# Optimization experiments

Measured on AMD Instinct MI355X. Metric: run time of the kernel, lower is better.

## Reference

```python
import jax, jax.numpy as jnp
import numpy as np

BATCH = 4096
INPUT_SIZE = 512
MAX_TERMS = 8
NUM_HEADS = 4
KERNEL_SIZE = 8  # must equal MAX_TERMS for the original module's math to be consistent
LN_EPS = 1e-5


def setup_inputs() -> dict:
    key = jax.random.key(0)
    k = jax.random.split(key, 6)
    x = jax.random.normal(k[0], (BATCH, INPUT_SIZE), dtype=jnp.float32)
    scale_param = jnp.ones((INPUT_SIZE,), dtype=jnp.float32)
    # ParameterList of num_heads tensors -> stacked along leading head dim
    poly_weights = jax.random.normal(k[1], (NUM_HEADS, INPUT_SIZE, MAX_TERMS), dtype=jnp.float32)
    kernels = jax.random.normal(k[2], (NUM_HEADS, INPUT_SIZE, MAX_TERMS, KERNEL_SIZE), dtype=jnp.float32)
    ln_gamma = jnp.ones((INPUT_SIZE * MAX_TERMS * NUM_HEADS,), dtype=jnp.float32)
    ln_beta = jnp.zeros((INPUT_SIZE * MAX_TERMS * NUM_HEADS,), dtype=jnp.float32)
    return {"x": x, "scale_param": scale_param, "poly_weights": poly_weights,
            "kernels": kernels, "ln_gamma": ln_gamma, "ln_beta": ln_beta}


def reference(x, scale_param, poly_weights, kernels, ln_gamma, ln_beta):
    b = x.shape[0]
    m = kernels.shape[2]  # max_terms
    xs = x * scale_param  # [b, i]
    # Chebyshev recurrence T_0..T_{m-1}; small fixed-length Python loop
    Ts = [jnp.ones_like(xs), xs]
    for _ in range(2, m):
        Ts.append(2.0 * xs * Ts[-1] - Ts[-2])
    x_cheb = jnp.stack(Ts, axis=-1)  # [b, i, m]
    # per-feature batched matmul over all heads at once: [b,h,i,k]
    x_head = jnp.einsum('bim,himk->bhik', x_cheb, kernels)
    # poly_weights broadcast (valid since k == m)
    x_head = x_head * poly_weights[None]  # [b,h,i,k]
    x_head = jax.nn.silu(x_head)
    # torch concatenates per-head flats along dim 1 -> (h, i, k) ordering
    flat = x_head.reshape(b, -1)  # [b, h*i*k]
    # LayerNorm (biased variance, eps=1e-5) over full feature dim
    mean = jnp.mean(flat, axis=-1, keepdims=True)
    var = jnp.mean(jnp.square(flat - mean), axis=-1, keepdims=True)
    out = (flat - mean) * jax.lax.rsqrt(var + LN_EPS) * ln_gamma + ln_beta
    return out
```

## Files before the change

### kernel.cpp

```cpp
#include <hip/hip_runtime.h>

#define BATCH 4096
#define ISZ   512
#define MT    8
#define NH    4
#define KS    8
#define NFEAT (NH * ISZ * KS)
#define LN_EPS 1e-5f

typedef float vfloat4 __attribute__((ext_vector_type(4)));

__global__ void prep_w2(const float* __restrict__ kern, const float* __restrict__ poly,
                        float* __restrict__ W2) {
    int dst = blockIdx.x * 256 + threadIdx.x;
    int l = dst & 3;
    int t = (dst >> 2) & 511;
    int q = (dst >> 11) & 7;
    int j = dst >> 14;
    int c = q >> 1;
    int m = (q & 1) * 4 + l;
    int f = j * 2048 + t * 4 + c;
    W2[dst] = kern[(f >> 3) * 64 + m * 8 + (f & 7)] * poly[f];
}

__device__ __forceinline__ float dot8(float4 w0, float4 w1, float4 a0, float4 a1) {
    return w0.x*a0.x + w0.y*a0.y + w0.z*a0.z + w0.w*a0.w
         + w1.x*a1.x + w1.y*a1.y + w1.z*a1.z + w1.w*a1.w;
}

__device__ __forceinline__ float fast_silu(float d) {
    return d * __builtin_amdgcn_rcpf(1.f + __expf(-d));
}

__device__ __forceinline__ void cheb_basis(float xs, float4& a0, float4& a1) {
    float t2x = xs + xs;
    a0.x = 1.f;
    a0.y = xs;
    a0.z = t2x * a0.y - a0.x;
    a0.w = t2x * a0.z - a0.y;
    a1.x = t2x * a0.w - a0.z;
    a1.y = t2x * a1.x - a0.w;
    a1.z = t2x * a1.y - a1.x;
    a1.w = t2x * a1.z - a1.y;
}

template <bool USE_W2>
__global__ __launch_bounds__(512)
void cheb_main(const float* __restrict__ x, const float* __restrict__ scale,
               const float4* __restrict__ W2v, const float* __restrict__ kern,
               const float* __restrict__ poly,
               const float* __restrict__ gamma, const float* __restrict__ beta,
               float* __restrict__ out) {
    __shared__ float xs[2][ISZ];
    __shared__ float red[8][4];

    const int t  = threadIdx.x;
    const int r0 = blockIdx.x * 2;

    for (int idx = t; idx < 2 * ISZ; idx += 512) {
        int r = idx >> 9, i = idx & 511;
        xs[r][i] = x[(r0 + r) * ISZ + i] * scale[i];
    }
    __syncthreads();

    float sum0 = 0.f, sq0 = 0.f, sum1 = 0.f, sq1 = 0.f;
    #pragma unroll
    for (int j = 0; j < 8; ++j) {
        const int i = (j * 256 + (t >> 1)) & 511;
        float4 wa[8];
        if (USE_W2) {
            #pragma unroll
            for (int q = 0; q < 8; ++q) wa[q] = W2v[(j * 8 + q) * 512 + t];
        } else {
            #pragma unroll
            for (int c = 0; c < 4; ++c) {
                const int f = j * 2048 + t * 4 + c;
                const float p = poly[f];
                const int base = (f >> 3) * 64 + (f & 7);
                wa[2*c]   = make_float4(kern[base]*p,    kern[base+8]*p,
                                        kern[base+16]*p, kern[base+24]*p);
                wa[2*c+1] = make_float4(kern[base+32]*p, kern[base+40]*p,
                                        kern[base+48]*p, kern[base+56]*p);
            }
        }
        float xa = xs[0][i], xb = xs[1][i];
        float4 a0, a1, b0, b1;
        cheb_basis(xa, a0, a1);
        cheb_basis(xb, b0, b1);
        #pragma unroll
        for (int c = 0; c < 4; ++c) {
            float s0 = fast_silu(dot8(wa[2*c], wa[2*c+1], a0, a1));
            float s1 = fast_silu(dot8(wa[2*c], wa[2*c+1], b0, b1));
            sum0 += s0; sq0 += s0 * s0;
            sum1 += s1; sq1 += s1 * s1;
        }
    }

    #pragma unroll
    for (int off = 32; off > 0; off >>= 1) {
        sum0 += __shfl_xor(sum0, off, 64);
        sq0  += __shfl_xor(sq0,  off, 64);
        sum1 += __shfl_xor(sum1, off, 64);
        sq1  += __shfl_xor(sq1,  off, 64);
    }
    const int wave = t >> 6;
    if ((t & 63) == 0) {
        red[wave][0] = sum0; red[wave][1] = sq0;
        red[wave][2] = sum1; red[wave][3] = sq1;
    }
    __syncthreads();

    float ts0 = 0.f, tq0 = 0.f, ts1 = 0.f, tq1 = 0.f;
    #pragma unroll
    for (int wv = 0; wv < 8; ++wv) {
        ts0 += red[wv][0]; tq0 += red[wv][1];
        ts1 += red[wv][2]; tq1 += red[wv][3];
    }
    const float invN = 1.f / (float)NFEAT;
    const float mean0 = ts0 * invN, mean1 = ts1 * invN;
    const float rs0 = rsqrtf(fmaxf(tq0 * invN - mean0 * mean0, 0.f) + LN_EPS);
    const float rs1 = rsqrtf(fmaxf(tq1 * invN - mean1 * mean1, 0.f) + LN_EPS);

    float* o0 = out + (size_t)r0 * NFEAT;
    float* o1 = o0 + NFEAT;
    #pragma unroll
    for (int j = 0; j < 8; ++j) {
        const int i  = (j * 256 + (t >> 1)) & 511;
        const int f0 = j * 2048 + t * 4;
        float4 wa[8];
        if (USE_W2) {
            #pragma unroll
            for (int q = 0; q < 8; ++q) wa[q] = W2v[(j * 8 + q) * 512 + t];
        } else {
            #pragma unroll
            for (int c = 0; c < 4; ++c) {
                const int f = f0 + c;
                const float p = poly[f];
                const int base = (f >> 3) * 64 + (f & 7);
                wa[2*c]   = make_float4(kern[base]*p,    kern[base+8]*p,
                                        kern[base+16]*p, kern[base+24]*p);
                wa[2*c+1] = make_float4(kern[base+32]*p, kern[base+40]*p,
                                        kern[base+48]*p, kern[base+56]*p);
            }
        }
        float xa = xs[0][i], xb = xs[1][i];
        float4 a0, a1, b0, b1;
        cheb_basis(xa, a0, a1);
        cheb_basis(xb, b0, b1);
        float4 g  = *(const float4*)(gamma + f0);
        float4 bb = *(const float4*)(beta  + f0);
        vfloat4 r0v, r1v;
        {
            float s;
            s = fast_silu(dot8(wa[0], wa[1], a0, a1));
            r0v.x = (s - mean0) * rs0 * g.x + bb.x;
            s = fast_silu(dot8(wa[2], wa[3], a0, a1));
            r0v.y = (s - mean0) * rs0 * g.y + bb.y;
            s = fast_silu(dot8(wa[4], wa[5], a0, a1));
            r0v.z = (s - mean0) * rs0 * g.z + bb.z;
            s = fast_silu(dot8(wa[6], wa[7], a0, a1));
            r0v.w = (s - mean0) * rs0 * g.w + bb.w;

            s = fast_silu(dot8(wa[0], wa[1], b0, b1));
            r1v.x = (s - mean1) * rs1 * g.x + bb.x;
            s = fast_silu(dot8(wa[2], wa[3], b0, b1));
            r1v.y = (s - mean1) * rs1 * g.y + bb.y;
            s = fast_silu(dot8(wa[4], wa[5], b0, b1));
            r1v.z = (s - mean1) * rs1 * g.z + bb.z;
            s = fast_silu(dot8(wa[6], wa[7], b0, b1));
            r1v.w = (s - mean1) * rs1 * g.w + bb.w;
        }
        __builtin_nontemporal_store(r0v, (vfloat4*)(o0 + f0));
        __builtin_nontemporal_store(r1v, (vfloat4*)(o1 + f0));
    }
}

extern "C" void kernel_launch(void* const* d_in, const int* in_sizes, int n_in,
                              void* d_out, int out_size, void* d_ws, size_t ws_size,
                              hipStream_t stream) {
    const float* x     = (const float*)d_in[0];
    const float* scale = (const float*)d_in[1];
    const float* poly  = (const float*)d_in[2];
    const float* kern  = (const float*)d_in[3];
    const float* gamma = (const float*)d_in[4];
    const float* beta  = (const float*)d_in[5];
    float* out = (float*)d_out;

    const size_t W2_BYTES = (size_t)NFEAT * 8 * sizeof(float);
    if (ws_size >= W2_BYTES) {
        float* W2 = (float*)d_ws;
        prep_w2<<<(NFEAT * 8) / 256, 256, 0, stream>>>(kern, poly, W2);
        cheb_main<true><<<BATCH / 2, 512, 0, stream>>>(x, scale, (const float4*)W2,
                                                       kern, poly, gamma, beta, out);
    } else {
        cheb_main<false><<<BATCH / 2, 512, 0, stream>>>(x, scale, nullptr,
                                                        kern, poly, gamma, beta, out);
    }
}
```

Before: 356.5 us.

## Convert Chebyshev weights to monomial form, use Horner, process four rows per block

```diff
diff --git a/kernel.cpp b/kernel.cpp
--- a/kernel.cpp
+++ b/kernel.cpp
@@ -7,66 +7,81 @@
 #define KS    8
 #define NFEAT (NH * ISZ * KS)
 #define LN_EPS 1e-5f
+#define ROWS  4
 
 typedef float vfloat4 __attribute__((ext_vector_type(4)));
 
+__device__ __forceinline__ void cheb2mono(const float w[8], float4& m0, float4& m1) {
+    m0.x = w[0] - w[2] + w[4] - w[6];
+    m0.y = w[1] - 3.f*w[3] + 5.f*w[5] - 7.f*w[7];
+    m0.z = 2.f*w[2] - 8.f*w[4] + 18.f*w[6];
+    m0.w = 4.f*w[3] - 20.f*w[5] + 56.f*w[7];
+    m1.x = 8.f*w[4] - 48.f*w[6];
+    m1.y = 16.f*w[5] - 112.f*w[7];
+    m1.z = 32.f*w[6];
+    m1.w = 64.f*w[7];
+}
+
 __global__ void prep_w2(const float* __restrict__ kern, const float* __restrict__ poly,
-                        float* __restrict__ W2) {
-    int dst = blockIdx.x * 256 + threadIdx.x;
-    int l = dst & 3;
-    int t = (dst >> 2) & 511;
-    int q = (dst >> 11) & 7;
-    int j = dst >> 14;
-    int c = q >> 1;
-    int m = (q & 1) * 4 + l;
-    int f = j * 2048 + t * 4 + c;
-    W2[dst] = kern[(f >> 3) * 64 + m * 8 + (f & 7)] * poly[f];
-}
-
-__device__ __forceinline__ float dot8(float4 w0, float4 w1, float4 a0, float4 a1) {
-    return w0.x*a0.x + w0.y*a0.y + w0.z*a0.z + w0.w*a0.w
-         + w1.x*a1.x + w1.y*a1.y + w1.z*a1.z + w1.w*a1.w;
+                        float4* __restrict__ W2) {
+    const int f = blockIdx.x * 256 + threadIdx.x;
+    const int j = f >> 11;
+    const int t = (f >> 2) & 511;
+    const int c = f & 3;
+    const int base = (f >> 3) * 64 + (f & 7);
+    const float p = poly[f];
+    float w[8];
+    #pragma unroll
+    for (int m = 0; m < 8; ++m) w[m] = kern[base + m * 8] * p;
+    float4 m0, m1;
+    cheb2mono(w, m0, m1);
+    W2[(j * 8 + 2 * c    ) * 512 + t] = m0;
+    W2[(j * 8 + 2 * c + 1) * 512 + t] = m1;
 }
 
 __device__ __forceinline__ float fast_silu(float d) {
     return d * __builtin_amdgcn_rcpf(1.f + __expf(-d));
 }
 
-__device__ __forceinline__ void cheb_basis(float xs, float4& a0, float4& a1) {
-    float t2x = xs + xs;
-    a0.x = 1.f;
-    a0.y = xs;
-    a0.z = t2x * a0.y - a0.x;
-    a0.w = t2x * a0.z - a0.y;
-    a1.x = t2x * a0.w - a0.z;
-    a1.y = t2x * a1.x - a0.w;
-    a1.z = t2x * a1.y - a1.x;
-    a1.w = t2x * a1.z - a1.y;
+__device__ __forceinline__ float horner8(float4 w0, float4 w1, float x) {
+    float s = w1.w;
+    s = fmaf(s, x, w1.z);
+    s = fmaf(s, x, w1.y);
+    s = fmaf(s, x, w1.x);
+    s = fmaf(s, x, w0.w);
+    s = fmaf(s, x, w0.z);
+    s = fmaf(s, x, w0.y);
+    s = fmaf(s, x, w0.x);
+    return s;
 }
 
 template <bool USE_W2>
-__global__ __launch_bounds__(512)
+__global__ __launch_bounds__(512, 4)
 void cheb_main(const float* __restrict__ x, const float* __restrict__ scale,
                const float4* __restrict__ W2v, const float* __restrict__ kern,
                const float* __restrict__ poly,
                const float* __restrict__ gamma, const float* __restrict__ beta,
                float* __restrict__ out) {
-    __shared__ float xs[2][ISZ];
-    __shared__ float red[8][4];
+    __shared__ float xs[ROWS][ISZ];
+    __shared__ float red[8][2 * ROWS];
 
     const int t  = threadIdx.x;
-    const int r0 = blockIdx.x * 2;
-
-    for (int idx = t; idx < 2 * ISZ; idx += 512) {
-        int r = idx >> 9, i = idx & 511;
+    const int r0 = blockIdx.x * ROWS;
+
+    #pragma unroll
+    for (int idx = t; idx < ROWS * ISZ; idx += 512) {
+        const int r = idx >> 9, i = idx & 511;
         xs[r][i] = x[(r0 + r) * ISZ + i] * scale[i];
     }
     __syncthreads();
 
-    float sum0 = 0.f, sq0 = 0.f, sum1 = 0.f, sq1 = 0.f;
+    float sum[ROWS], sq[ROWS];
+    #pragma unroll
+    for (int r = 0; r < ROWS; ++r) { sum[r] = 0.f; sq[r] = 0.f; }
+
     #pragma unroll
     for (int j = 0; j < 8; ++j) {
-        const int i = (j * 256 + (t >> 1)) & 511;
+        const int i = ((j & 1) << 8) + (t >> 1);
         float4 wa[8];
         if (USE_W2) {
             #pragma unroll
@@ -75,57 +90,63 @@
             #pragma unroll
             for (int c = 0; c < 4; ++c) {
                 const int f = j * 2048 + t * 4 + c;
+                const int base = (f >> 3) * 64 + (f & 7);
                 const float p = poly[f];
-                const int base = (f >> 3) * 64 + (f & 7);
-                wa[2*c]   = make_float4(kern[base]*p,    kern[base+8]*p,
-                                        kern[base+16]*p, kern[base+24]*p);
-                wa[2*c+1] = make_float4(kern[base+32]*p, kern[base+40]*p,
-                                        kern[base+48]*p, kern[base+56]*p);
-            }
-        }
-        float xa = xs[0][i], xb = xs[1][i];
-        float4 a0, a1, b0, b1;
-        cheb_basis(xa, a0, a1);
-        cheb_basis(xb, b0, b1);
+                float w[8];
+                #pragma unroll
+                for (int m = 0; m < 8; ++m) w[m] = kern[base + m * 8] * p;
+                cheb2mono(w, wa[2 * c], wa[2 * c + 1]);
+            }
+        }
+        float xv[ROWS];
+        #pragma unroll
+        for (int r = 0; r < ROWS; ++r) xv[r] = xs[r][i];
         #pragma unroll
         for (int c = 0; c < 4; ++c) {
-            float s0 = fast_silu(dot8(wa[2*c], wa[2*c+1], a0, a1));
-            float s1 = fast_silu(dot8(wa[2*c], wa[2*c+1], b0, b1));
-            sum0 += s0; sq0 += s0 * s0;
-            sum1 += s1; sq1 += s1 * s1;
+            #pragma unroll
+            for (int r = 0; r < ROWS; ++r) {
+                const float s = fast_silu(horner8(wa[2 * c], wa[2 * c + 1], xv[r]));
+                sum[r] += s;
+                sq[r]   = fmaf(s, s, sq[r]);
+            }
         }
     }
 
     #pragma unroll
     for (int off = 32; off > 0; off >>= 1) {
-        sum0 += __shfl_xor(sum0, off, 64);
-        sq0  += __shfl_xor(sq0,  off, 64);
-        sum1 += __shfl_xor(sum1, off, 64);
-        sq1  += __shfl_xor(sq1,  off, 64);
+        #pragma unroll
+        for (int r = 0; r < ROWS; ++r) {
+            sum[r] += __shfl_xor(sum[r], off, 64);
+            sq[r]  += __shfl_xor(sq[r],  off, 64);
+        }
     }
     const int wave = t >> 6;
     if ((t & 63) == 0) {
-        red[wave][0] = sum0; red[wave][1] = sq0;
-        red[wave][2] = sum1; red[wave][3] = sq1;
+        #pragma unroll
+        for (int r = 0; r < ROWS; ++r) {
+            red[wave][r]        = sum[r];
+            red[wave][ROWS + r] = sq[r];
+        }
     }
     __syncthreads();
 
-    float ts0 = 0.f, tq0 = 0.f, ts1 = 0.f, tq1 = 0.f;
-    #pragma unroll
-    for (int wv = 0; wv < 8; ++wv) {
-        ts0 += red[wv][0]; tq0 += red[wv][1];
-        ts1 += red[wv][2]; tq1 += red[wv][3];
-    }
-    const float invN = 1.f / (float)NFEAT;
-    const float mean0 = ts0 * invN, mean1 = ts1 * invN;
-    const float rs0 = rsqrtf(fmaxf(tq0 * invN - mean0 * mean0, 0.f) + LN_EPS);
-    const float rs1 = rsqrtf(fmaxf(tq1 * invN - mean1 * mean1, 0.f) + LN_EPS);
-
-    float* o0 = out + (size_t)r0 * NFEAT;
-    float* o1 = o0 + NFEAT;
+    float rs[ROWS], nm[ROWS];
+    {
+        const float invN = 1.f / (float)NFEAT;
+        #pragma unroll
+        for (int r = 0; r < ROWS; ++r) {
+            float ts = 0.f, tq = 0.f;
+            #pragma unroll
+            for (int wv = 0; wv < 8; ++wv) { ts += red[wv][r]; tq += red[wv][ROWS + r]; }
+            const float mean = ts * invN;
+            rs[r] = rsqrtf(fmaxf(tq * invN - mean * mean, 0.f) + LN_EPS);
+            nm[r] = -mean * rs[r];
+        }
+    }
+
     #pragma unroll
     for (int j = 0; j < 8; ++j) {
-        const int i  = (j * 256 + (t >> 1)) & 511;
+        const int i  = ((j & 1) << 8) + (t >> 1);
         const int f0 = j * 2048 + t * 4;
         float4 wa[8];
         if (USE_W2) {
@@ -135,43 +156,34 @@
             #pragma unroll
             for (int c = 0; c < 4; ++c) {
                 const int f = f0 + c;
+                const int base = (f >> 3) * 64 + (f & 7);
                 const float p = poly[f];
-                const int base = (f >> 3) * 64 + (f & 7);
-                wa[2*c]   = make_float4(kern[base]*p,    kern[base+8]*p,
-                                        kern[base+16]*p, kern[base+24]*p);
-                wa[2*c+1] = make_float4(kern[base+32]*p, kern[base+40]*p,
-                                        kern[base+48]*p, kern[base+56]*p);
-            }
-        }
-        float xa = xs[0][i], xb = xs[1][i];
-        float4 a0, a1, b0, b1;
-        cheb_basis(xa, a0, a1);
-        cheb_basis(xb, b0, b1);
-        float4 g  = *(const float4*)(gamma + f0);
-        float4 bb = *(const float4*)(beta  + f0);
-        vfloat4 r0v, r1v;
-        {
-            float s;
-            s = fast_silu(dot8(wa[0], wa[1], a0, a1));
-            r0v.x = (s - mean0) * rs0 * g.x + bb.x;
-            s = fast_silu(dot8(wa[2], wa[3], a0, a1));
-            r0v.y = (s - mean0) * rs0 * g.y + bb.y;
-            s = fast_silu(dot8(wa[4], wa[5], a0, a1));
-            r0v.z = (s - mean0) * rs0 * g.z + bb.z;
-            s = fast_silu(dot8(wa[6], wa[7], a0, a1));
-            r0v.w = (s - mean0) * rs0 * g.w + bb.w;
-
-            s = fast_silu(dot8(wa[0], wa[1], b0, b1));
-            r1v.x = (s - mean1) * rs1 * g.x + bb.x;
-            s = fast_silu(dot8(wa[2], wa[3], b0, b1));
-            r1v.y = (s - mean1) * rs1 * g.y + bb.y;
-            s = fast_silu(dot8(wa[4], wa[5], b0, b1));
-            r1v.z = (s - mean1) * rs1 * g.z + bb.z;
-            s = fast_silu(dot8(wa[6], wa[7], b0, b1));
-            r1v.w = (s - mean1) * rs1 * g.w + bb.w;
-        }
-        __builtin_nontemporal_store(r0v, (vfloat4*)(o0 + f0));
-        __builtin_nontemporal_store(r1v, (vfloat4*)(o1 + f0));
+                float w[8];
+                #pragma unroll
+                for (int m = 0; m < 8; ++m) w[m] = kern[base + m * 8] * p;
+                cheb2mono(w, wa[2 * c], wa[2 * c + 1]);
+            }
+        }
+        float xv[ROWS];
+        #pragma unroll
+        for (int r = 0; r < ROWS; ++r) xv[r] = xs[r][i];
+        const float4 g  = *(const float4*)(gamma + f0);
+        const float4 bb = *(const float4*)(beta  + f0);
+        vfloat4 rv[ROWS];
+        #pragma unroll
+        for (int c = 0; c < 4; ++c) {
+            const float gc = (c == 0) ? g.x  : (c == 1) ? g.y  : (c == 2) ? g.z  : g.w;
+            const float bc = (c == 0) ? bb.x : (c == 1) ? bb.y : (c == 2) ? bb.z : bb.w;
+            #pragma unroll
+            for (int r = 0; r < ROWS; ++r) {
+                const float s = fast_silu(horner8(wa[2 * c], wa[2 * c + 1], xv[r]));
+                rv[r][c] = fmaf(fmaf(s, rs[r], nm[r]), gc, bc);
+            }
+        }
+        #pragma unroll
+        for (int r = 0; r < ROWS; ++r)
+            __builtin_nontemporal_store(rv[r],
+                (vfloat4*)(out + (size_t)(r0 + r) * NFEAT + f0));
     }
 }
 
@@ -188,12 +200,12 @@
 
     const size_t W2_BYTES = (size_t)NFEAT * 8 * sizeof(float);
     if (ws_size >= W2_BYTES) {
-        float* W2 = (float*)d_ws;
-        prep_w2<<<(NFEAT * 8) / 256, 256, 0, stream>>>(kern, poly, W2);
-        cheb_main<true><<<BATCH / 2, 512, 0, stream>>>(x, scale, (const float4*)W2,
-                                                       kern, poly, gamma, beta, out);
+        float4* W2 = (float4*)d_ws;
+        prep_w2<<<NFEAT / 256, 256, 0, stream>>>(kern, poly, W2);
+        cheb_main<true><<<BATCH / ROWS, 512, 0, stream>>>(x, scale, (const float4*)W2,
+                                                          kern, poly, gamma, beta, out);
     } else {
-        cheb_main<false><<<BATCH / 2, 512, 0, stream>>>(x, scale, nullptr,
-                                                        kern, poly, gamma, beta, out);
-    }
-}
+        cheb_main<false><<<BATCH / ROWS, 512, 0, stream>>>(x, scale, nullptr,
+                                                           kern, poly, gamma, beta, out);
+    }
+}
```

Result: no change. 353.5 us (median of 2 runs) (-0.8%).
